# Kernel optimization log

Measured on AMD Instinct MI355X. Metric: run time of the kernel, lower is better.

Reference implementation:

```python
import jax, jax.numpy as jnp
import numpy as np

NEG = -1000000.0  # mask value used by the original module


def setup_inputs() -> dict:
    key = jax.random.key(0)
    ks = jax.random.split(key, 8)
    N, D_IN, D_Q, D_K, E = 8192, 512, 512, 512, 262144
    s = 1.0 / np.sqrt(D_IN)
    return {
        "x": jax.random.normal(ks[0], (N, D_IN), dtype=jnp.float32),
        "edge_index": jax.random.randint(ks[1], (2, E), 0, N, dtype=jnp.int64),
        "Wq": jax.random.normal(ks[2], (D_IN, D_Q), dtype=jnp.float32) * s,
        "bq": jax.random.normal(ks[3], (D_Q,), dtype=jnp.float32) * 0.01,
        "Wk": jax.random.normal(ks[4], (D_IN, D_K), dtype=jnp.float32) * s,
        "bk": jax.random.normal(ks[5], (D_K,), dtype=jnp.float32) * 0.01,
        "Wv": jax.random.normal(ks[6], (D_IN, D_K), dtype=jnp.float32) * s,
        "bv": jax.random.normal(ks[7], (D_K,), dtype=jnp.float32) * 0.01,
    }


def reference(x, edge_index, Wq, bq, Wk, bk, Wv, bv):
    # Linear projections (x: [N, D_in])
    q = x @ Wq + bq  # [N, Dq]
    k = x @ Wk + bk  # [N, Dk]
    v = x @ Wv + bv  # [N, Dk]

    N = x.shape[0]
    # Dense adjacency from edge list (matches torch scatter adjacency[e0, e1] = 1)
    adj = jnp.zeros((N, N), dtype=x.dtype).at[edge_index[0], edge_index[1]].set(1.0)

    # Full scores (ptr=None branch), scaled by sqrt(Dq)
    a = (q @ k.T) / jnp.sqrt(jnp.asarray(q.shape[-1], dtype=x.dtype))
    a = a * adj + (1.0 - adj) * NEG

    attn = jax.nn.softmax(a, axis=-1)  # [N, N]
    return attn @ v  # [N, Dk]
```

## Files before the change

### kernel.cpp

```cpp
#include <hip/hip_runtime.h>


#define N_NODES 8192
#define DIM 512
#define MASK_WORDS 256
#define CAPW 512

typedef __attribute__((ext_vector_type(8))) short short8;
typedef __attribute__((ext_vector_type(4))) float f32x4;

__device__ __forceinline__ unsigned short f2bf(float f) {
    unsigned int u = __float_as_uint(f);
    u += 0x7fffu + ((u >> 16) & 1u);
    return (unsigned short)(u >> 16);
}
__device__ __forceinline__ float bf_lo(unsigned int w) { return __uint_as_float(w << 16); }
__device__ __forceinline__ float bf_hi(unsigned int w) { return __uint_as_float(w & 0xffff0000u); }

__device__ __forceinline__ float wred_sum(float s) {
    #pragma unroll
    for (int off = 1; off <= 32; off <<= 1) s += __shfl_xor(s, off, 64);
    return s;
}
__device__ __forceinline__ int wred_sumi(int s) {
    #pragma unroll
    for (int off = 1; off <= 32; off <<= 1) s += __shfl_xor(s, off, 64);
    return s;
}
__device__ __forceinline__ float dot8(uint4 a, uint4 b) {
    return bf_lo(a.x) * bf_lo(b.x) + bf_hi(a.x) * bf_hi(b.x)
         + bf_lo(a.y) * bf_lo(b.y) + bf_hi(a.y) * bf_hi(b.y)
         + bf_lo(a.z) * bf_lo(b.z) + bf_hi(a.z) * bf_hi(b.z)
         + bf_lo(a.w) * bf_lo(b.w) + bf_hi(a.w) * bf_hi(b.w);
}

__global__ __launch_bounds__(256) void prep1(
    const float* __restrict__ x, unsigned short* __restrict__ xb,
    const float* __restrict__ Wq, const float* __restrict__ Wk,
    const float* __restrict__ Wv, unsigned short* __restrict__ Wt,
    unsigned int* __restrict__ mask)
{
    __shared__ float sm[32][33];
    const int b = blockIdx.x;
    if (b < 4096) {
        int i = b * 256 + threadIdx.x;
        float4 f = ((const float4*)x)[i];
        ushort4 o;
        o.x = f2bf(f.x); o.y = f2bf(f.y); o.z = f2bf(f.z); o.w = f2bf(f.w);
        ((ushort4*)xb)[i] = o;
        ((uint2*)mask)[i] = make_uint2(0u, 0u);
    } else {
        int bb = b - 4096;
        int which = bb >> 8, t = bb & 255;
        const float* __restrict__ W = (which == 0) ? Wq : (which == 1) ? Wk : Wv;
        unsigned short* __restrict__ outp = Wt + (size_t)which * DIM * DIM;
        int n0 = (t & 15) * 32, k0 = (t >> 4) * 32;
        int tx = threadIdx.x & 31, ty = threadIdx.x >> 5;
        #pragma unroll
        for (int r = 0; r < 4; ++r)
            sm[ty + 8 * r][tx] = W[(size_t)(k0 + ty + 8 * r) * DIM + n0 + tx];
        __syncthreads();
        #pragma unroll
        for (int r = 0; r < 4; ++r)
            outp[(size_t)(n0 + ty + 8 * r) * DIM + k0 + tx] = f2bf(sm[tx][ty + 8 * r]);
    }
}

__global__ __launch_bounds__(256) void prep2(
    const int* __restrict__ ei, unsigned int* __restrict__ mask, int E)
{
    int e = blockIdx.x * 256 + threadIdx.x;
    if (e >= E) return;
    int src = ei[e];
    int dst = ei[E + e];
    atomicOr(&mask[(size_t)src * MASK_WORDS + (dst >> 5)], 1u << (dst & 31));
}

__device__ __forceinline__ void load_lds16(const unsigned short* g, unsigned short* l) {
    __builtin_amdgcn_global_load_lds(
        (const __attribute__((address_space(1))) unsigned int*)g,
        (__attribute__((address_space(3))) unsigned int*)l, 16, 0, 0);
}

__global__ __launch_bounds__(256) void mfma_gemm(
    const unsigned short* __restrict__ xb, const unsigned short* __restrict__ Wt,
    const float* __restrict__ bq, const float* __restrict__ bk, const float* __restrict__ bv,
    unsigned short* __restrict__ qkv)
{
    const int p = blockIdx.x;
    const int xcd = p & 7;
    const int s = p >> 3;
    const int mloc = s / 12;
    const int n = s - 12 * mloc;
    const int which = n >> 2;
    const int row0 = (xcd * 8 + mloc) << 7;
    const int col0 = (n & 3) << 7;

    const unsigned short* __restrict__ Bm = Wt + (size_t)which * DIM * DIM;
    const float* __restrict__ bias = (which == 0) ? bq : (which == 1) ? bk : bv;
    unsigned short* __restrict__ outp = qkv + (size_t)which * N_NODES * DIM;

    const int tid = threadIdx.x;
    const int lane = tid & 63;
    const int w = tid >> 6;
    const int wm = (w >> 1) * 64;
    const int wn = (w & 1) * 64;
    const int L = lane & 15;
    const int quad = lane >> 4;

    __shared__ unsigned short smem[16384];
    unsigned short* Aw = smem + w * 4096;
    unsigned short* Bw = Aw + 2048;

    f32x4 zero = {0.f, 0.f, 0.f, 0.f};
    f32x4 acc[4][4];
    #pragma unroll
    for (int i = 0; i < 4; ++i)
        #pragma unroll
        for (int j = 0; j < 4; ++j) acc[i][j] = zero;

    int gm[4], gko[4];
    #pragma unroll
    for (int t = 0; t < 4; ++t) {
        int chunk = t * 64 + lane;
        gm[t] = chunk >> 2;
        gko[t] = ((chunk & 3) ^ (gm[t] & 3)) << 3;
    }
    const unsigned short* arow = xb + (size_t)(row0 + wm) * DIM;
    const unsigned short* brow = Bm + (size_t)(col0 + wn) * DIM;

    for (int k0 = 0; k0 < DIM; k0 += 32) {
        __builtin_amdgcn_s_waitcnt(0);
        #pragma unroll
        for (int t = 0; t < 4; ++t)
            load_lds16(arow + (size_t)gm[t] * DIM + k0 + gko[t], Aw + t * 512);
        #pragma unroll
        for (int t = 0; t < 4; ++t)
            load_lds16(brow + (size_t)gm[t] * DIM + k0 + gko[t], Bw + t * 512);
        __builtin_amdgcn_s_waitcnt(0);
        __builtin_amdgcn_sched_barrier(0);

        short8 a[4], bfr[4];
        #pragma unroll
        for (int i = 0; i < 4; ++i) {
            int r = i * 16 + L;
            a[i] = *(const short8*)(const void*)&Aw[r * 32 + ((quad ^ (r & 3)) << 3)];
        }
        #pragma unroll
        for (int j = 0; j < 4; ++j) {
            int r = j * 16 + L;
            bfr[j] = *(const short8*)(const void*)&Bw[r * 32 + ((quad ^ (r & 3)) << 3)];
        }

        #pragma unroll
        for (int i = 0; i < 4; ++i)
            #pragma unroll
            for (int j = 0; j < 4; ++j)
                acc[i][j] = __builtin_amdgcn_mfma_f32_16x16x32_bf16(a[i], bfr[j], acc[i][j], 0, 0, 0);
        __builtin_amdgcn_sched_barrier(0);
    }

    float biasv[4];
    #pragma unroll
    for (int j = 0; j < 4; ++j) biasv[j] = bias[col0 + wn + j * 16 + L];

    unsigned short* tb = smem;
    #pragma unroll
    for (int round = 0; round < 2; ++round) {
        __syncthreads();
        if ((w >> 1) == round) {
            #pragma unroll
            for (int i = 0; i < 4; ++i)
                #pragma unroll
                for (int j = 0; j < 4; ++j)
                    #pragma unroll
                    for (int r = 0; r < 4; ++r)
                        tb[(i * 16 + quad * 4 + r) * 128 + wn + j * 16 + L] =
                            f2bf(acc[i][j][r] + biasv[j]);
        }
        __syncthreads();
        const int rrow = tid >> 2;
        const int seg = (tid & 3) * 32;
        const uint4* srcv = (const uint4*)&tb[rrow * 128 + seg];
        unsigned short* dst = outp + (size_t)(row0 + round * 64 + rrow) * DIM + col0 + seg;
        #pragma unroll
        for (int ss = 0; ss < 4; ++ss)
            *(uint4*)(dst + ss * 8) = srcv[ss];
    }
}

__device__ __forceinline__ void fused_pass(
    const unsigned short* __restrict__ k, const unsigned short* __restrict__ v,
    const unsigned short* nbrw, int cn, uint4 qv, int lane,
    float* o, float& l_run)
{
    const float scale = 0.044194173824159220f;
    for (int p0 = 0; p0 < cn; p0 += 4) {
        int j0 = nbrw[p0];
        int j1 = nbrw[(p0 + 1 < cn) ? p0 + 1 : p0];
        int j2 = nbrw[(p0 + 2 < cn) ? p0 + 2 : p0];
        int j3 = nbrw[(p0 + 3 < cn) ? p0 + 3 : p0];
        uint4 k0v = *(const uint4*)(k + (size_t)j0 * DIM + lane * 8);
        uint4 k1v = *(const uint4*)(k + (size_t)j1 * DIM + lane * 8);
        uint4 k2v = *(const uint4*)(k + (size_t)j2 * DIM + lane * 8);
        uint4 k3v = *(const uint4*)(k + (size_t)j3 * DIM + lane * 8);
        uint4 v0 = *(const uint4*)(v + (size_t)j0 * DIM + lane * 8);
        uint4 v1 = *(const uint4*)(v + (size_t)j1 * DIM + lane * 8);
        uint4 v2 = *(const uint4*)(v + (size_t)j2 * DIM + lane * 8);
        uint4 v3 = *(const uint4*)(v + (size_t)j3 * DIM + lane * 8);
        float s0 = wred_sum(dot8(qv, k0v));
        float s1 = wred_sum(dot8(qv, k1v));
        float s2 = wred_sum(dot8(qv, k2v));
        float s3 = wred_sum(dot8(qv, k3v));
        float w0 = __expf(s0 * scale);
        float w1 = (p0 + 1 < cn) ? __expf(s1 * scale) : 0.f;
        float w2 = (p0 + 2 < cn) ? __expf(s2 * scale) : 0.f;
        float w3 = (p0 + 3 < cn) ? __expf(s3 * scale) : 0.f;
        l_run += w0 + w1 + w2 + w3;
        o[0] += w0 * bf_lo(v0.x) + w1 * bf_lo(v1.x) + w2 * bf_lo(v2.x) + w3 * bf_lo(v3.x);
        o[1] += w0 * bf_hi(v0.x) + w1 * bf_hi(v1.x) + w2 * bf_hi(v2.x) + w3 * bf_hi(v3.x);
        o[2] += w0 * bf_lo(v0.y) + w1 * bf_lo(v1.y) + w2 * bf_lo(v2.y) + w3 * bf_lo(v3.y);
        o[3] += w0 * bf_hi(v0.y) + w1 * bf_hi(v1.y) + w2 * bf_hi(v2.y) + w3 * bf_hi(v3.y);
        o[4] += w0 * bf_lo(v0.z) + w1 * bf_lo(v1.z) + w2 * bf_lo(v2.z) + w3 * bf_lo(v3.z);
        o[5] += w0 * bf_hi(v0.z) + w1 * bf_hi(v1.z) + w2 * bf_hi(v2.z) + w3 * bf_hi(v3.z);
        o[6] += w0 * bf_lo(v0.w) + w1 * bf_lo(v1.w) + w2 * bf_lo(v2.w) + w3 * bf_lo(v3.w);
        o[7] += w0 * bf_hi(v0.w) + w1 * bf_hi(v1.w) + w2 * bf_hi(v2.w) + w3 * bf_hi(v3.w);
    }
}

__device__ __forceinline__ int wave_excl_scan(int pc, int lane) {
    int incl = pc;
    #pragma unroll
    for (int off = 1; off <= 32; off <<= 1) {
        int nv = __shfl_up(incl, off, 64);
        if (lane >= off) incl += nv;
    }
    return incl;
}

__global__ __launch_bounds__(256) void attn_kernel(
    const unsigned short* __restrict__ q, const unsigned short* __restrict__ k,
    const unsigned short* __restrict__ v, const unsigned int* __restrict__ mask,
    float* __restrict__ out)
{
    __shared__ unsigned short nbr[4][CAPW];

    const int tid = threadIdx.x;
    const int lane = tid & 63;
    const int wid = tid >> 6;
    const int row = blockIdx.x * 4 + wid;

    const uint4 qv = *(const uint4*)(q + (size_t)row * DIM + lane * 8);
    const unsigned int* __restrict__ mrow = mask + (size_t)row * MASK_WORDS;

    const uint4 mv = ((const uint4*)mrow)[lane];
    unsigned int wds[4] = {mv.x, mv.y, mv.z, mv.w};
    int pc = __popc(wds[0]) + __popc(wds[1]) + __popc(wds[2]) + __popc(wds[3]);
    const int total = wred_sumi(pc);

    float o[8];
    #pragma unroll
    for (int i = 0; i < 8; ++i) o[i] = 0.f;

    if (total == 0) {
        for (int j = 0; j < N_NODES; ++j) {
            uint4 vv = *(const uint4*)(v + (size_t)j * DIM + lane * 8);
            o[0] += bf_lo(vv.x); o[1] += bf_hi(vv.x);
            o[2] += bf_lo(vv.y); o[3] += bf_hi(vv.y);
            o[4] += bf_lo(vv.z); o[5] += bf_hi(vv.z);
            o[6] += bf_lo(vv.w); o[7] += bf_hi(vv.w);
        }
        const float sc = 1.0f / N_NODES;
        float4 r0 = {o[0] * sc, o[1] * sc, o[2] * sc, o[3] * sc};
        float4 r1 = {o[4] * sc, o[5] * sc, o[6] * sc, o[7] * sc};
        *(float4*)(out + (size_t)row * DIM + lane * 8) = r0;
        *(float4*)(out + (size_t)row * DIM + lane * 8 + 4) = r1;
        return;
    }

    float l_run = 0.f;

    if (total <= CAPW) {
        int pos = wave_excl_scan(pc, lane) - pc;
        #pragma unroll
        for (int t = 0; t < 4; ++t) {
            unsigned int ww = wds[t];
            int base = (lane * 4 + t) * 32;
            while (ww) {
                int b = __ffs(ww) - 1; ww &= ww - 1;
                nbr[wid][pos++] = (unsigned short)(base + b);
            }
        }
        fused_pass(k, v, nbr[wid], total, qv, lane, o, l_run);
    } else {
        for (int c = 0; c < 16; ++c) {
            unsigned int ww = 0;
            if (lane < 16) ww = mrow[c * 16 + lane];
            int pcc = __popc(ww);
            int incl = wave_excl_scan(pcc, lane);
            int cn = __shfl(incl, 63, 64);
            if (cn == 0) continue;
            int pos = incl - pcc;
            int base = (c * 16 + lane) * 32;
            while (ww) {
                int b = __ffs(ww) - 1; ww &= ww - 1;
                nbr[wid][pos++] = (unsigned short)(base + b);
            }
            fused_pass(k, v, nbr[wid], cn, qv, lane, o, l_run);
        }
    }

    const float inv = 1.0f / l_run;
    float4 r0 = {o[0] * inv, o[1] * inv, o[2] * inv, o[3] * inv};
    float4 r1 = {o[4] * inv, o[5] * inv, o[6] * inv, o[7] * inv};
    *(float4*)(out + (size_t)row * DIM + lane * 8) = r0;
    *(float4*)(out + (size_t)row * DIM + lane * 8 + 4) = r1;
}

extern "C" void kernel_launch(void* const* d_in, const int* in_sizes, int n_in,
                              void* d_out, int out_size, void* d_ws, size_t ws_size,
                              hipStream_t stream)
{
    const float* x  = (const float*)d_in[0];
    const int*   ei = (const int*)d_in[1];
    const float* Wq = (const float*)d_in[2];
    const float* bq = (const float*)d_in[3];
    const float* Wk = (const float*)d_in[4];
    const float* bk = (const float*)d_in[5];
    const float* Wv = (const float*)d_in[6];
    const float* bv = (const float*)d_in[7];
    float* out = (float*)d_out;

    const int E = in_sizes[1] / 2;
    const size_t NM = (size_t)N_NODES * DIM;

    unsigned short* xb = (unsigned short*)d_ws;
    unsigned short* Wt = xb + NM;
    unsigned short* qkv = Wt + (size_t)3 * DIM * DIM;
    unsigned short* qb = qkv;
    unsigned short* kb = qkv + NM;
    unsigned short* vb = qkv + 2 * NM;
    unsigned int* mask = (unsigned int*)(qkv + 3 * NM);

    prep1<<<4864, 256, 0, stream>>>(x, xb, Wq, Wk, Wv, Wt, mask);
    prep2<<<(E + 255) / 256, 256, 0, stream>>>(ei, mask, E);

    mfma_gemm<<<768, 256, 0, stream>>>(xb, Wt, bq, bk, bv, qkv);

    attn_kernel<<<N_NODES / 4, 256, 0, stream>>>(qb, kb, vb, mask, out);
}
```

Measured before the change: 187.0 us.

## Interleave K/V rows, fuse edge scatter into GEMM launch, drop LDS staging

K and V are written into a single interleaved buffer with a 1024-element row stride, so each neighbor's key and value sit next to each other for the gather in the attention kernel. The edge-to-bitmask scatter becomes extra blocks of the GEMM launch, which removes one kernel launch and lets the scatter overlap with the matrix multiply. The GEMM no longer stages operands in LDS and instead loads MFMA fragments straight from global memory with a 2x unrolled loop. That removes the LDS copy and waits but may cost global load efficiency and reuse.

Result: slower. 202.5 us (+8.3%).

```diff
diff --git a/kernel.cpp b/kernel.cpp
--- a/kernel.cpp
+++ b/kernel.cpp
@@ -5,6 +5,7 @@
 #define DIM 512
 #define MASK_WORDS 256
 #define CAPW 512
+#define KV_STRIDE 1024
 
 typedef __attribute__((ext_vector_type(8))) short short8;
 typedef __attribute__((ext_vector_type(4))) float f32x4;
@@ -66,27 +67,26 @@
     }
 }
 
-__global__ __launch_bounds__(256) void prep2(
-    const int* __restrict__ ei, unsigned int* __restrict__ mask, int E)
-{
-    int e = blockIdx.x * 256 + threadIdx.x;
-    if (e >= E) return;
-    int src = ei[e];
-    int dst = ei[E + e];
-    atomicOr(&mask[(size_t)src * MASK_WORDS + (dst >> 5)], 1u << (dst & 31));
-}
-
-__device__ __forceinline__ void load_lds16(const unsigned short* g, unsigned short* l) {
-    __builtin_amdgcn_global_load_lds(
-        (const __attribute__((address_space(1))) unsigned int*)g,
-        (__attribute__((address_space(3))) unsigned int*)l, 16, 0, 0);
-}
-
-__global__ __launch_bounds__(256) void mfma_gemm(
+__global__ __launch_bounds__(256) void gemm_scatter(
     const unsigned short* __restrict__ xb, const unsigned short* __restrict__ Wt,
     const float* __restrict__ bq, const float* __restrict__ bk, const float* __restrict__ bv,
-    unsigned short* __restrict__ qkv)
-{
+    unsigned short* __restrict__ qb, unsigned short* __restrict__ kv,
+    const int* __restrict__ ei, unsigned int* __restrict__ mask, int E)
+{
+    __shared__ unsigned short tb[64 * 128];
+
+    const int tid = threadIdx.x;
+
+    if (blockIdx.x >= 768) {
+        int e = (blockIdx.x - 768) * 256 + tid;
+        if (e < E) {
+            int src = ei[e];
+            int dst = ei[E + e];
+            atomicOr(&mask[(size_t)src * MASK_WORDS + (dst >> 5)], 1u << (dst & 31));
+        }
+        return;
+    }
+
     const int p = blockIdx.x;
     const int xcd = p & 7;
     const int s = p >> 3;
@@ -98,9 +98,10 @@
 
     const unsigned short* __restrict__ Bm = Wt + (size_t)which * DIM * DIM;
     const float* __restrict__ bias = (which == 0) ? bq : (which == 1) ? bk : bv;
-    unsigned short* __restrict__ outp = qkv + (size_t)which * N_NODES * DIM;
-
-    const int tid = threadIdx.x;
+    unsigned short* __restrict__ obase =
+        (which == 0) ? qb : (which == 1) ? kv : kv + DIM;
+    const size_t ostride = (which == 0) ? DIM : KV_STRIDE;
+
     const int lane = tid & 63;
     const int w = tid >> 6;
     const int wm = (w >> 1) * 64;
@@ -108,10 +109,6 @@
     const int L = lane & 15;
     const int quad = lane >> 4;
 
-    __shared__ unsigned short smem[16384];
-    unsigned short* Aw = smem + w * 4096;
-    unsigned short* Bw = Aw + 2048;
-
     f32x4 zero = {0.f, 0.f, 0.f, 0.f};
     f32x4 acc[4][4];
     #pragma unroll
@@ -119,52 +116,29 @@
         #pragma unroll
         for (int j = 0; j < 4; ++j) acc[i][j] = zero;
 
-    int gm[4], gko[4];
-    #pragma unroll
-    for (int t = 0; t < 4; ++t) {
-        int chunk = t * 64 + lane;
-        gm[t] = chunk >> 2;
-        gko[t] = ((chunk & 3) ^ (gm[t] & 3)) << 3;
-    }
-    const unsigned short* arow = xb + (size_t)(row0 + wm) * DIM;
-    const unsigned short* brow = Bm + (size_t)(col0 + wn) * DIM;
-
+    const unsigned short* __restrict__ ab = xb + (size_t)(row0 + wm + L) * DIM + quad * 8;
+    const unsigned short* __restrict__ bb = Bm + (size_t)(col0 + wn + L) * DIM + quad * 8;
+
+    #pragma unroll 2
     for (int k0 = 0; k0 < DIM; k0 += 32) {
-        __builtin_amdgcn_s_waitcnt(0);
-        #pragma unroll
-        for (int t = 0; t < 4; ++t)
-            load_lds16(arow + (size_t)gm[t] * DIM + k0 + gko[t], Aw + t * 512);
-        #pragma unroll
-        for (int t = 0; t < 4; ++t)
-            load_lds16(brow + (size_t)gm[t] * DIM + k0 + gko[t], Bw + t * 512);
-        __builtin_amdgcn_s_waitcnt(0);
-        __builtin_amdgcn_sched_barrier(0);
-
         short8 a[4], bfr[4];
         #pragma unroll
-        for (int i = 0; i < 4; ++i) {
-            int r = i * 16 + L;
-            a[i] = *(const short8*)(const void*)&Aw[r * 32 + ((quad ^ (r & 3)) << 3)];
-        }
-        #pragma unroll
-        for (int j = 0; j < 4; ++j) {
-            int r = j * 16 + L;
-            bfr[j] = *(const short8*)(const void*)&Bw[r * 32 + ((quad ^ (r & 3)) << 3)];
-        }
-
+        for (int i = 0; i < 4; ++i)
+            a[i] = *(const short8*)(const void*)(ab + (size_t)i * 16 * DIM + k0);
+        #pragma unroll
+        for (int j = 0; j < 4; ++j)
+            bfr[j] = *(const short8*)(const void*)(bb + (size_t)j * 16 * DIM + k0);
         #pragma unroll
         for (int i = 0; i < 4; ++i)
             #pragma unroll
             for (int j = 0; j < 4; ++j)
                 acc[i][j] = __builtin_amdgcn_mfma_f32_16x16x32_bf16(a[i], bfr[j], acc[i][j], 0, 0, 0);
-        __builtin_amdgcn_sched_barrier(0);
     }
 
     float biasv[4];
     #pragma unroll
     for (int j = 0; j < 4; ++j) biasv[j] = bias[col0 + wn + j * 16 + L];
 
-    unsigned short* tb = smem;
     #pragma unroll
     for (int round = 0; round < 2; ++round) {
         __syncthreads();
@@ -182,7 +156,8 @@
         const int rrow = tid >> 2;
         const int seg = (tid & 3) * 32;
         const uint4* srcv = (const uint4*)&tb[rrow * 128 + seg];
-        unsigned short* dst = outp + (size_t)(row0 + round * 64 + rrow) * DIM + col0 + seg;
+        unsigned short* dst =
+            obase + (size_t)(row0 + round * 64 + rrow) * ostride + col0 + seg;
         #pragma unroll
         for (int ss = 0; ss < 4; ++ss)
             *(uint4*)(dst + ss * 8) = srcv[ss];
@@ -190,7 +165,7 @@
 }
 
 __device__ __forceinline__ void fused_pass(
-    const unsigned short* __restrict__ k, const unsigned short* __restrict__ v,
+    const unsigned short* __restrict__ kv,
     const unsigned short* nbrw, int cn, uint4 qv, int lane,
     float* o, float& l_run)
 {
@@ -200,14 +175,18 @@
         int j1 = nbrw[(p0 + 1 < cn) ? p0 + 1 : p0];
         int j2 = nbrw[(p0 + 2 < cn) ? p0 + 2 : p0];
         int j3 = nbrw[(p0 + 3 < cn) ? p0 + 3 : p0];
-        uint4 k0v = *(const uint4*)(k + (size_t)j0 * DIM + lane * 8);
-        uint4 k1v = *(const uint4*)(k + (size_t)j1 * DIM + lane * 8);
-        uint4 k2v = *(const uint4*)(k + (size_t)j2 * DIM + lane * 8);
-        uint4 k3v = *(const uint4*)(k + (size_t)j3 * DIM + lane * 8);
-        uint4 v0 = *(const uint4*)(v + (size_t)j0 * DIM + lane * 8);
-        uint4 v1 = *(const uint4*)(v + (size_t)j1 * DIM + lane * 8);
-        uint4 v2 = *(const uint4*)(v + (size_t)j2 * DIM + lane * 8);
-        uint4 v3 = *(const uint4*)(v + (size_t)j3 * DIM + lane * 8);
+        const unsigned short* n0p = kv + (size_t)j0 * KV_STRIDE + lane * 8;
+        const unsigned short* n1p = kv + (size_t)j1 * KV_STRIDE + lane * 8;
+        const unsigned short* n2p = kv + (size_t)j2 * KV_STRIDE + lane * 8;
+        const unsigned short* n3p = kv + (size_t)j3 * KV_STRIDE + lane * 8;
+        uint4 k0v = *(const uint4*)n0p;
+        uint4 k1v = *(const uint4*)n1p;
+        uint4 k2v = *(const uint4*)n2p;
+        uint4 k3v = *(const uint4*)n3p;
+        uint4 v0 = *(const uint4*)(n0p + DIM);
+        uint4 v1 = *(const uint4*)(n1p + DIM);
+        uint4 v2 = *(const uint4*)(n2p + DIM);
+        uint4 v3 = *(const uint4*)(n3p + DIM);
         float s0 = wred_sum(dot8(qv, k0v));
         float s1 = wred_sum(dot8(qv, k1v));
         float s2 = wred_sum(dot8(qv, k2v));
@@ -228,7 +207,7 @@
     }
 }
 
-__device__ __forceinline__ int wave_excl_scan(int pc, int lane) {
+__device__ __forceinline__ int wave_incl_scan(int pc, int lane) {
     int incl = pc;
     #pragma unroll
     for (int off = 1; off <= 32; off <<= 1) {
@@ -239,9 +218,8 @@
 }
 
 __global__ __launch_bounds__(256) void attn_kernel(
-    const unsigned short* __restrict__ q, const unsigned short* __restrict__ k,
-    const unsigned short* __restrict__ v, const unsigned int* __restrict__ mask,
-    float* __restrict__ out)
+    const unsigned short* __restrict__ q, const unsigned short* __restrict__ kv,
+    const unsigned int* __restrict__ mask, float* __restrict__ out)
 {
     __shared__ unsigned short nbr[4][CAPW];
 
@@ -264,7 +242,7 @@
 
     if (total == 0) {
         for (int j = 0; j < N_NODES; ++j) {
-            uint4 vv = *(const uint4*)(v + (size_t)j * DIM + lane * 8);
+            uint4 vv = *(const uint4*)(kv + (size_t)j * KV_STRIDE + DIM + lane * 8);
             o[0] += bf_lo(vv.x); o[1] += bf_hi(vv.x);
             o[2] += bf_lo(vv.y); o[3] += bf_hi(vv.y);
             o[4] += bf_lo(vv.z); o[5] += bf_hi(vv.z);
@@ -281,7 +259,7 @@
     float l_run = 0.f;
 
     if (total <= CAPW) {
-        int pos = wave_excl_scan(pc, lane) - pc;
+        int pos = wave_incl_scan(pc, lane) - pc;
         #pragma unroll
         for (int t = 0; t < 4; ++t) {
             unsigned int ww = wds[t];
@@ -291,13 +269,13 @@
                 nbr[wid][pos++] = (unsigned short)(base + b);
             }
         }
-        fused_pass(k, v, nbr[wid], total, qv, lane, o, l_run);
+        fused_pass(kv, nbr[wid], total, qv, lane, o, l_run);
     } else {
         for (int c = 0; c < 16; ++c) {
             unsigned int ww = 0;
             if (lane < 16) ww = mrow[c * 16 + lane];
             int pcc = __popc(ww);
-            int incl = wave_excl_scan(pcc, lane);
+            int incl = wave_incl_scan(pcc, lane);
             int cn = __shfl(incl, 63, 64);
             if (cn == 0) continue;
             int pos = incl - pcc;
@@ -306,7 +284,7 @@
                 int b = __ffs(ww) - 1; ww &= ww - 1;
                 nbr[wid][pos++] = (unsigned short)(base + b);
             }
-            fused_pass(k, v, nbr[wid], cn, qv, lane, o, l_run);
+            fused_pass(kv, nbr[wid], cn, qv, lane, o, l_run);
         }
     }
 
@@ -336,16 +314,14 @@
 
     unsigned short* xb = (unsigned short*)d_ws;
     unsigned short* Wt = xb + NM;
-    unsigned short* qkv = Wt + (size_t)3 * DIM * DIM;
-    unsigned short* qb = qkv;
-    unsigned short* kb = qkv + NM;
-    unsigned short* vb = qkv + 2 * NM;
-    unsigned int* mask = (unsigned int*)(qkv + 3 * NM);
+    unsigned short* qb = Wt + (size_t)3 * DIM * DIM;
+    unsigned short* kv = qb + NM;
+    unsigned int* mask = (unsigned int*)(kv + (size_t)N_NODES * KV_STRIDE);
 
     prep1<<<4864, 256, 0, stream>>>(x, xb, Wq, Wk, Wv, Wt, mask);
-    prep2<<<(E + 255) / 256, 256, 0, stream>>>(ei, mask, E);
-
-    mfma_gemm<<<768, 256, 0, stream>>>(xb, Wt, bq, bk, bv, qkv);
-
-    attn_kernel<<<N_NODES / 4, 256, 0, stream>>>(qb, kb, vb, mask, out);
-}
+
+    gemm_scatter<<<768 + (E + 255) / 256, 256, 0, stream>>>(
+        xb, Wt, bq, bk, bv, qb, kv, ei, mask, E);
+
+    attn_kernel<<<N_NODES / 4, 256, 0, stream>>>(qb, kv, mask, out);
+}
```
